# Performance work log

Measured on AMD Instinct MI355X. Metric: run time of the kernel, lower is better.

## Reference

```python
import jax, jax.numpy as jnp
import numpy as np

NS, B, PH = 8, 1024, 12
XS, ZS, RNN = 256, 32, 512
LS, LPS = 8, 2           # len_state, len_pred_state
IN = LPS + ZS + XS       # GRU input size (include_robot=False)
DT = 0.4                 # SingleIntegrator dt


def setup_inputs() -> dict:
    key = jax.random.key(0)
    ks = jax.random.split(key, 16)
    g = lambda k, sh, s=0.05: jax.random.normal(k, sh, dtype=jnp.float32) * s
    N = NS * B
    return {
        "x": g(ks[0], (B, XS), 1.0),
        "x_r_t0": g(ks[1], (B, LS), 1.0),
        "z_stacked": g(ks[2], (NS, B, ZS), 1.0),
        "p0": g(ks[3], (B, 2), 1.0),
        "eps_step": g(ks[4], (PH, N, 2), 1.0),
        "eps_final": g(ks[5], (NS, B, PH, 2), 1.0),
        "W_sa": g(ks[6], (LPS, LS)), "b_sa": jnp.zeros((LPS,), jnp.float32),
        "W_ih": g(ks[7], (3 * RNN, IN)), "b_ih": jnp.zeros((3 * RNN,), jnp.float32),
        "W_hh": g(ks[8], (3 * RNN, RNN)), "b_hh": jnp.zeros((3 * RNN,), jnp.float32),
        "W_h0": g(ks[9], (RNN, ZS + XS)), "b_h0": jnp.zeros((RNN,), jnp.float32),
        "W_mu": g(ks[10], (LPS, RNN)), "b_mu": jnp.zeros((LPS,), jnp.float32),
        "W_ls": g(ks[11], (LPS, RNN), 0.01), "b_ls": jnp.zeros((LPS,), jnp.float32),
        "W_corr": g(ks[12], (1, RNN), 0.01), "b_corr": jnp.zeros((1,), jnp.float32),
        "prediction_horizon": PH,
        "n_samples": NS,
    }


def _gmm_sample(mus, log_sigmas, rho, eps):
    # Reparameterized sample from a single-component 2D correlated Gaussian:
    # a = mu + L @ eps with L = [[sx, 0], [sy*rho, sy*sqrt(1-rho^2)]]
    s = jnp.exp(log_sigmas)
    dx = s[..., 0] * eps[..., 0]
    dy = s[..., 1] * (rho * eps[..., 0]
                      + jnp.sqrt(jnp.clip(1.0 - rho * rho, 1e-5, None)) * eps[..., 1])
    return mus + jnp.stack([dx, dy], axis=-1)


def reference(x, x_r_t0, z_stacked, p0, eps_step, eps_final,
              W_sa, b_sa, W_ih, b_ih, W_hh, b_hh, W_h0, b_h0,
              W_mu, b_mu, W_ls, b_ls, W_corr, b_corr,
              prediction_horizon, n_samples):
    ns, bsz, zs = z_stacked.shape
    z = z_stacked.reshape(-1, zs)                               # [N, z]
    zx = jnp.concatenate([z, jnp.tile(x, (n_samples, 1))], axis=1)  # [N, z+x]
    state0 = zx @ W_h0.T + b_h0                                 # initial_h
    a0 = jnp.tile(x_r_t0 @ W_sa.T + b_sa, (n_samples, 1))       # state_action

    def step(carry, eps_t):
        h, a = carry
        inp = jnp.concatenate([zx, a], axis=1)                  # [N, IN]
        gi = inp @ W_ih.T + b_ih
        gh = h @ W_hh.T + b_hh
        ir, iz, inn = jnp.split(gi, 3, axis=1)
        hr, hz, hn = jnp.split(gh, 3, axis=1)
        r = jax.nn.sigmoid(ir + hr)
        u = jax.nn.sigmoid(iz + hz)
        n = jnp.tanh(inn + r * hn)
        h_new = (1.0 - u) * n + u * h                           # GRUCell
        mus = h_new @ W_mu.T + b_mu                             # [N, 2]
        log_sigmas = h_new @ W_ls.T + b_ls                      # [N, 2]
        corrs = jnp.tanh(h_new @ W_corr.T + b_corr)[:, 0]       # [N]
        a_t = _gmm_sample(mus, log_sigmas, corrs, eps_t)        # gmm.rsample()
        return (h_new, a_t), (mus, log_sigmas, corrs)

    _, (mus, log_sigmas, corrs) = jax.lax.scan(step, (state0, a0), eps_step)
    # [PH, N, .] -> [n_samples, B, PH, .]  (n_components == 1)
    mus = mus.transpose(1, 0, 2).reshape(n_samples, bsz, prediction_horizon, 2)
    log_sigmas = log_sigmas.transpose(1, 0, 2).reshape(n_samples, bsz, prediction_horizon, 2)
    corrs = corrs.transpose(1, 0).reshape(n_samples, bsz, prediction_horizon, 1)
    log_pis = jnp.ones_like(corrs)                              # ones_like path (n_components==1)

    # a_dist.rsample() then SingleIntegrator.integrate_samples
    a_sample = _gmm_sample(mus, log_sigmas, corrs[..., 0], eps_final)
    preds = jnp.cumsum(a_sample, axis=2) * DT + p0[None, :, None, :]
    return (log_pis, mus, log_sigmas, corrs, preds)
```

## Files before the change

kernel.cpp:

```cpp
#include <hip/hip_runtime.h>
#include <hip/hip_bf16.h>
#include <math.h>

#define NSAMP 8
#define BATCH 1024
#define PH 12
#define XS 256
#define ZS 32
#define RNN 512
#define LSZ 8
#define INP 290
#define NTOT 8192
#define DT 0.4f

#define LOGPI_OFF 0
#define MUS_OFF   (NTOT*PH)
#define LSIG_OFF  (MUS_OFF + NTOT*PH*2)
#define CORR_OFF  (LSIG_OFF + NTOT*PH*2)
#define PRED_OFF  (CORR_OFF + NTOT*PH)

typedef float f32x4 __attribute__((ext_vector_type(4)));
typedef __bf16 bf16x8 __attribute__((ext_vector_type(8)));

__device__ __forceinline__ float sigmoid_(float x) {
    return 1.0f / (1.0f + __expf(-x));
}
__device__ __forceinline__ float tanh_(float x) {
    return 1.0f - 2.0f / (__expf(2.0f * x) + 1.0f);
}

__device__ __forceinline__ void async16(const void* g, void* l) {
    __builtin_amdgcn_global_load_lds((const __attribute__((address_space(1))) void*)g,
                                     (__attribute__((address_space(3))) void*)l, 16, 0, 0);
}


__global__ void k_init_a(const float* __restrict__ x_r_t0,
                         const float* __restrict__ W_sa,
                         const float* __restrict__ b_sa,
                         float* __restrict__ a) {
    int n = blockIdx.x * blockDim.x + threadIdx.x;
    if (n >= NTOT) return;
    int b = n & (BATCH - 1);
    float a0 = b_sa[0], a1 = b_sa[1];
#pragma unroll
    for (int k = 0; k < LSZ; ++k) {
        float xv = x_r_t0[b * LSZ + k];
        a0 = fmaf(xv, W_sa[0 * LSZ + k], a0);
        a1 = fmaf(xv, W_sa[1 * LSZ + k], a1);
    }
    a[n * 2 + 0] = a0;
    a[n * 2 + 1] = a1;
}

__global__ void k_cast_zx(const float* __restrict__ z, const float* __restrict__ x,
                          __hip_bfloat16* __restrict__ zx) {
    int n = blockIdx.x, k = threadIdx.x;
    if (k >= 288) return;
    float v = (k < 32) ? z[n * ZS + k] : x[(n & (BATCH - 1)) * XS + (k - 32)];
    zx[(size_t)n * 288 + k] = __float2bfloat16(v);
}

__global__ void k_cast_w(const float* __restrict__ W_h0, const float* __restrict__ W_ih,
                         __hip_bfloat16* __restrict__ Wcat) {
    int r = blockIdx.x, k = threadIdx.x;
    if (k >= 288) return;
    float v = (r < RNN) ? W_h0[r * 288 + k] : W_ih[(size_t)(r - RNN) * INP + k];
    Wcat[(size_t)r * 288 + k] = __float2bfloat16(v);
}

__global__ void k_cast_whh(const float* __restrict__ W, __hip_bfloat16* __restrict__ Wb) {
    int i = blockIdx.x * 256 + threadIdx.x;
    Wb[i] = __float2bfloat16(W[i]);
}

__global__ __launch_bounds__(256, 2) void k_gemm0_mfma(
    const __hip_bfloat16* __restrict__ zx, const __hip_bfloat16* __restrict__ Wcat,
    const float* __restrict__ b_h0, const float* __restrict__ b_ih,
    __hip_bfloat16* __restrict__ h0, __hip_bfloat16* __restrict__ gi)
{
    __shared__ __align__(16) char sA[8192];
    __shared__ __align__(16) char sB[8192];
    const int tid = threadIdx.x;
    const int wv = tid >> 6, lane = tid & 63;
    const int fq = lane >> 4, fr = lane & 15;
    const int wr = wv >> 1, wc = wv & 1;
    const int tile_r = blockIdx.x * 128, tile_c = blockIdx.y * 128;

    f32x4 acc[4][4];
#pragma unroll
    for (int i = 0; i < 4; ++i)
#pragma unroll
        for (int j = 0; j < 4; ++j) acc[i][j] = (f32x4){0.f, 0.f, 0.f, 0.f};

    for (int k0 = 0; k0 < 288; k0 += 32) {
#pragma unroll
        for (int j = 0; j < 2; ++j) {
            int ck = wv * 2 + j;
            int row = ck * 16 + (lane >> 2);
            int slot = lane & 3;
            async16(zx + (size_t)(tile_r + row) * 288 + k0 + ((slot ^ (row & 3)) << 3),
                    sA + ck * 1024 + lane * 16);
        }
#pragma unroll
        for (int j = 0; j < 2; ++j) {
            int ck = wv * 2 + j;
            int row = ck * 16 + (lane >> 2);
            int slot = lane & 3;
            async16(Wcat + (size_t)(tile_c + row) * 288 + k0 + ((slot ^ (row & 3)) << 3),
                    sB + ck * 1024 + lane * 16);
        }
        __syncthreads();
        bf16x8 af[4], bv[4];
#pragma unroll
        for (int i = 0; i < 4; ++i) {
            int r = wr * 64 + i * 16 + fr;
            af[i] = *(const bf16x8*)(sA + r * 64 + ((fq ^ (r & 3)) << 4));
        }
#pragma unroll
        for (int j = 0; j < 4; ++j) {
            int r = wc * 64 + j * 16 + fr;
            bv[j] = *(const bf16x8*)(sB + r * 64 + ((fq ^ (r & 3)) << 4));
        }
#pragma unroll
        for (int i = 0; i < 4; ++i)
#pragma unroll
            for (int j = 0; j < 4; ++j)
                acc[i][j] = __builtin_amdgcn_mfma_f32_16x16x32_bf16(af[i], bv[j], acc[i][j], 0, 0, 0);
        __syncthreads();
    }

#pragma unroll
    for (int jn = 0; jn < 4; ++jn) {
        int cg = tile_c + wc * 64 + jn * 16 + fr;
        float bias = (cg < RNN) ? b_h0[cg] : b_ih[cg - RNN];
#pragma unroll
        for (int i = 0; i < 4; ++i)
#pragma unroll
            for (int q = 0; q < 4; ++q) {
                int rg = tile_r + wr * 64 + i * 16 + fq * 4 + q;
                float v = acc[i][jn][q] + bias;
                if (cg < RNN) h0[(size_t)rg * RNN + cg] = __float2bfloat16(v);
                else          gi[(size_t)rg * 1536 + (cg - RNN)] = __float2bfloat16(v);
            }
    }
}

#define GRU_LDS_A 32768
#define GRU_LDS_BUF 57344
__global__ __launch_bounds__(512, 2) void k_gru_step_mfma(
    const __hip_bfloat16* __restrict__ h, const float* __restrict__ a,
    const __hip_bfloat16* __restrict__ gi,
    const __hip_bfloat16* __restrict__ Whh, const float* __restrict__ b_hh,
    const float* __restrict__ W_ih,
    __hip_bfloat16* __restrict__ h_new)
{
    __shared__ __align__(16) char lds[2][GRU_LDS_BUF];
    const int tid = threadIdx.x;
    const int wv = tid >> 6, lane = tid & 63;
    const int fq = lane >> 4, fr = lane & 15;
    const int wr = wv >> 1, wc = wv & 1;
    const int tile_r = blockIdx.x * 256;
    const int tile_c = blockIdx.y * 64;

    f32x4 acc[3][4][2];
#pragma unroll
    for (int g = 0; g < 3; ++g)
#pragma unroll
        for (int i = 0; i < 4; ++i)
#pragma unroll
            for (int j = 0; j < 2; ++j) acc[g][i][j] = (f32x4){0.f, 0.f, 0.f, 0.f};

    const int lrow = lane >> 2;
    const int slot = (lane & 3) ^ (lrow & 3);

    auto stage = [&](int b, int k0) {
#pragma unroll
        for (int j = 0; j < 7; ++j) {
            int c = wv * 7 + j;
            if (c < 32) {
                int rowgrp = c >> 1, kh = c & 1;
                int row = tile_r + rowgrp * 16 + lrow;
                async16(h + (size_t)row * RNN + k0 + kh * 32 + slot * 8,
                        lds[b] + c * 1024 + lane * 16);
            } else {
                int cp = c - 32;
                int grp = cp >> 1, kh = cp & 1;
                int rB = grp * 16 + lrow;
                int gate = rB >> 6, col = rB & 63;
                async16(Whh + (size_t)(gate * RNN + tile_c + col) * RNN + k0 + kh * 32 + slot * 8,
                        lds[b] + GRU_LDS_A + cp * 1024 + lane * 16);
            }
        }
    };

    auto compute = [&](int b) {
        const char* bufA = lds[b];
        const char* bufB = lds[b] + GRU_LDS_A;
        const int rsw = (fq ^ (fr & 3)) << 4;
#pragma unroll
        for (int ks = 0; ks < 2; ++ks) {
            bf16x8 af[4];
#pragma unroll
            for (int i = 0; i < 4; ++i) {
                int chunk = (wr * 4 + i) * 2 + ks;
                af[i] = *(const bf16x8*)(bufA + chunk * 1024 + fr * 64 + rsw);
            }
            bf16x8 bv[3][2];
#pragma unroll
            for (int g = 0; g < 3; ++g)
#pragma unroll
                for (int j = 0; j < 2; ++j) {
                    int grp = g * 4 + wc * 2 + j;
                    int chunk = grp * 2 + ks;
                    bv[g][j] = *(const bf16x8*)(bufB + chunk * 1024 + fr * 64 + rsw);
                }
#pragma unroll
            for (int g = 0; g < 3; ++g)
#pragma unroll
                for (int i = 0; i < 4; ++i)
#pragma unroll
                    for (int j = 0; j < 2; ++j)
                        acc[g][i][j] = __builtin_amdgcn_mfma_f32_16x16x32_bf16(
                            af[i], bv[g][j], acc[g][i][j], 0, 0, 0);
        }
    };

    stage(0, 0);
    __syncthreads();
    int buf = 0;
#pragma unroll 1
    for (int t = 0; t < 7; ++t) {
        stage(buf ^ 1, (t + 1) * 64);
        compute(buf);
        __syncthreads();
        buf ^= 1;
    }
    compute(buf);

#pragma unroll
    for (int j = 0; j < 2; ++j) {
        const int cg = tile_c + wc * 32 + j * 16 + fr;
        const float bh_r = b_hh[cg], bh_z = b_hh[RNN + cg], bh_n = b_hh[2 * RNN + cg];
        const float wr0 = W_ih[(size_t)cg * INP + 288],             wr1 = W_ih[(size_t)cg * INP + 289];
        const float wz0 = W_ih[(size_t)(RNN + cg) * INP + 288],     wz1 = W_ih[(size_t)(RNN + cg) * INP + 289];
        const float wn0 = W_ih[(size_t)(2 * RNN + cg) * INP + 288], wn1 = W_ih[(size_t)(2 * RNN + cg) * INP + 289];
#pragma unroll
        for (int i = 0; i < 4; ++i)
#pragma unroll
            for (int q = 0; q < 4; ++q) {
                const int rg = tile_r + wr * 64 + i * 16 + fq * 4 + q;
                const float2 av = *(const float2*)&a[rg * 2];
                const float gr = __bfloat162float(gi[(size_t)rg * 1536 + cg])
                                 + av.x * wr0 + av.y * wr1 + acc[0][i][j][q] + bh_r;
                const float gz = __bfloat162float(gi[(size_t)rg * 1536 + RNN + cg])
                                 + av.x * wz0 + av.y * wz1 + acc[1][i][j][q] + bh_z;
                const float gn = __bfloat162float(gi[(size_t)rg * 1536 + 2 * RNN + cg])
                                 + av.x * wn0 + av.y * wn1;
                const float r_ = sigmoid_(gr);
                const float u_ = sigmoid_(gz);
                const float n_ = tanh_(gn + r_ * (acc[2][i][j][q] + bh_n));
                const float hv = __bfloat162float(h[(size_t)rg * RNN + cg]);
                h_new[(size_t)rg * RNN + cg] = __float2bfloat16((1.0f - u_) * n_ + u_ * hv);
            }
    }
}

__global__ __launch_bounds__(256) void k_heads(
    const __hip_bfloat16* __restrict__ h_new,
    const float* __restrict__ W_mu, const float* __restrict__ b_mu,
    const float* __restrict__ W_ls, const float* __restrict__ b_ls,
    const float* __restrict__ W_corr, const float* __restrict__ b_corr,
    const float* __restrict__ eps_step_t,
    float* __restrict__ out, float* __restrict__ a, int t)
{
    const int wid = (blockIdx.x * blockDim.x + threadIdx.x) >> 6;
    const int lane = threadIdx.x & 63;
    if (wid >= NTOT) return;
    const int kbase = lane * 8;
    float hv[8];
    {
        uint4 v = *reinterpret_cast<const uint4*>(&h_new[(size_t)wid * RNN + kbase]);
        unsigned uu[4] = {v.x, v.y, v.z, v.w};
#pragma unroll
        for (int p = 0; p < 4; ++p) {
            hv[2 * p]     = __uint_as_float(uu[p] << 16);
            hv[2 * p + 1] = __uint_as_float(uu[p] & 0xffff0000u);
        }
    }
    float s0 = 0.f, s1 = 0.f, s2 = 0.f, s3 = 0.f, s4 = 0.f;
#pragma unroll
    for (int q = 0; q < 8; ++q) {
        int k = kbase + q;
        s0 = fmaf(hv[q], W_mu[k], s0);
        s1 = fmaf(hv[q], W_mu[RNN + k], s1);
        s2 = fmaf(hv[q], W_ls[k], s2);
        s3 = fmaf(hv[q], W_ls[RNN + k], s3);
        s4 = fmaf(hv[q], W_corr[k], s4);
    }
#pragma unroll
    for (int m = 32; m >= 1; m >>= 1) {
        s0 += __shfl_xor(s0, m, 64);
        s1 += __shfl_xor(s1, m, 64);
        s2 += __shfl_xor(s2, m, 64);
        s3 += __shfl_xor(s3, m, 64);
        s4 += __shfl_xor(s4, m, 64);
    }
    if (lane == 0) {
        const int n = wid;
        const float mu0 = s0 + b_mu[0], mu1 = s1 + b_mu[1];
        const float ls0 = s2 + b_ls[0], ls1 = s3 + b_ls[1];
        const float rho = tanh_(s4 + b_corr[0]);
        out[MUS_OFF + (n * PH + t) * 2 + 0] = mu0;
        out[MUS_OFF + (n * PH + t) * 2 + 1] = mu1;
        out[LSIG_OFF + (n * PH + t) * 2 + 0] = ls0;
        out[LSIG_OFF + (n * PH + t) * 2 + 1] = ls1;
        out[CORR_OFF + n * PH + t] = rho;
        const float e0 = eps_step_t[n * 2 + 0], e1 = eps_step_t[n * 2 + 1];
        const float sg0 = __expf(ls0), sg1 = __expf(ls1);
        a[n * 2 + 0] = mu0 + sg0 * e0;
        a[n * 2 + 1] = mu1 + sg1 * (rho * e0 + sqrtf(fmaxf(1e-5f, 1.0f - rho * rho)) * e1);
    }
}

__global__ void k_final(const float* __restrict__ p0,
                        const float* __restrict__ eps_final,
                        float* __restrict__ out)
{
    int n = blockIdx.x * blockDim.x + threadIdx.x;
    if (n >= NTOT) return;
    const int b = n & (BATCH - 1);
    const float px = p0[b * 2 + 0], py = p0[b * 2 + 1];
    float cx = 0.f, cy = 0.f;
#pragma unroll
    for (int t = 0; t < PH; ++t) {
        const float mu0 = out[MUS_OFF + (n * PH + t) * 2 + 0];
        const float mu1 = out[MUS_OFF + (n * PH + t) * 2 + 1];
        const float ls0 = out[LSIG_OFF + (n * PH + t) * 2 + 0];
        const float ls1 = out[LSIG_OFF + (n * PH + t) * 2 + 1];
        const float rho = out[CORR_OFF + n * PH + t];
        const float e0 = eps_final[(n * PH + t) * 2 + 0];
        const float e1 = eps_final[(n * PH + t) * 2 + 1];
        const float sg0 = __expf(ls0), sg1 = __expf(ls1);
        cx += mu0 + sg0 * e0;
        cy += mu1 + sg1 * (rho * e0 + sqrtf(fmaxf(1e-5f, 1.0f - rho * rho)) * e1);
        out[PRED_OFF + (n * PH + t) * 2 + 0] = cx * DT + px;
        out[PRED_OFF + (n * PH + t) * 2 + 1] = cy * DT + py;
        out[LOGPI_OFF + n * PH + t] = 1.0f;
    }
}

extern "C" void kernel_launch(void* const* d_in, const int* in_sizes, int n_in,
                              void* d_out, int out_size, void* d_ws, size_t ws_size,
                              hipStream_t stream) {
    const float* x        = (const float*)d_in[0];
    const float* x_r_t0   = (const float*)d_in[1];
    const float* z        = (const float*)d_in[2];
    const float* p0       = (const float*)d_in[3];
    const float* eps_step = (const float*)d_in[4];
    const float* eps_fin  = (const float*)d_in[5];
    const float* W_sa     = (const float*)d_in[6];
    const float* b_sa     = (const float*)d_in[7];
    const float* W_ih     = (const float*)d_in[8];
    const float* b_ih     = (const float*)d_in[9];
    const float* W_hh     = (const float*)d_in[10];
    const float* b_hh     = (const float*)d_in[11];
    const float* W_h0     = (const float*)d_in[12];
    const float* b_h0     = (const float*)d_in[13];
    const float* W_mu     = (const float*)d_in[14];
    const float* b_mu     = (const float*)d_in[15];
    const float* W_ls     = (const float*)d_in[16];
    const float* b_ls     = (const float*)d_in[17];
    const float* W_corr   = (const float*)d_in[18];
    const float* b_corr   = (const float*)d_in[19];

    char* wp = (char*)d_ws;
    float* a            = (float*)wp;          wp += (size_t)NTOT * 2 * 4;
    __hip_bfloat16* zxb = (__hip_bfloat16*)wp; wp += (size_t)NTOT * 288 * 2;
    __hip_bfloat16* Wcat= (__hip_bfloat16*)wp; wp += (size_t)2048 * 288 * 2;
    __hip_bfloat16* Whhb= (__hip_bfloat16*)wp; wp += (size_t)1536 * RNN * 2;
    __hip_bfloat16* h0  = (__hip_bfloat16*)wp; wp += (size_t)NTOT * RNN * 2;
    __hip_bfloat16* h1  = (__hip_bfloat16*)wp; wp += (size_t)NTOT * RNN * 2;
    __hip_bfloat16* gi  = (__hip_bfloat16*)wp; wp += (size_t)NTOT * 1536 * 2;
    float* out = (float*)d_out;

    k_init_a<<<dim3(NTOT / 256), dim3(256), 0, stream>>>(x_r_t0, W_sa, b_sa, a);
    k_cast_zx<<<dim3(NTOT), dim3(320), 0, stream>>>(z, x, zxb);
    k_cast_w<<<dim3(2048), dim3(320), 0, stream>>>(W_h0, W_ih, Wcat);
    k_cast_whh<<<dim3(1536 * RNN / 256), dim3(256), 0, stream>>>(W_hh, Whhb);
    k_gemm0_mfma<<<dim3(64, 16), dim3(256), 0, stream>>>(zxb, Wcat, b_h0, b_ih, h0, gi);

    __hip_bfloat16* hc = h0;
    __hip_bfloat16* hn = h1;
    for (int t = 0; t < PH; ++t) {
        k_gru_step_mfma<<<dim3(NTOT / 256, RNN / 64), dim3(512), 0, stream>>>(
            hc, a, gi, Whhb, b_hh, W_ih, hn);
        k_heads<<<dim3(NTOT * 64 / 256), dim3(256), 0, stream>>>(
            hn, W_mu, b_mu, W_ls, b_ls, W_corr, b_corr,
            eps_step + (size_t)t * NTOT * 2, out, a, t);
        __hip_bfloat16* tmp = hc; hc = hn; hn = tmp;
    }
    k_final<<<dim3(NTOT / 256), dim3(256), 0, stream>>>(p0, eps_fin, out);
}
```

Baseline: 422.5 us.

## Fuse head projections into GRU step epilogue via per-slice partial sums

The GRU step kernel now computes the mu, log-sigma and corr projections of the new hidden state in its epilogue. It reduces across the 16 columns of each fragment with shuffles and writes 16 per-slice partials per row to a workspace buffer. A light k_heads_fin kernel then sums the partials, applies biases, writes the outputs and samples the next action. This removes the extra pass that re-read the full bf16 hidden state every step, at the cost of more epilogue registers (launch bounds relaxed to 1 block) and an extra partials buffer round-trip.

```diff
diff --git a/kernel.cpp b/kernel.cpp
--- a/kernel.cpp
+++ b/kernel.cpp
@@ -148,12 +148,14 @@
 
 #define GRU_LDS_A 32768
 #define GRU_LDS_BUF 57344
-__global__ __launch_bounds__(512, 2) void k_gru_step_mfma(
+__global__ __launch_bounds__(512, 1) void k_gru_step_mfma(
     const __hip_bfloat16* __restrict__ h, const float* __restrict__ a,
     const __hip_bfloat16* __restrict__ gi,
     const __hip_bfloat16* __restrict__ Whh, const float* __restrict__ b_hh,
     const float* __restrict__ W_ih,
-    __hip_bfloat16* __restrict__ h_new)
+    const float* __restrict__ W_mu, const float* __restrict__ W_ls,
+    const float* __restrict__ W_corr,
+    __hip_bfloat16* __restrict__ h_new, float* __restrict__ partial)
 {
     __shared__ __align__(16) char lds[2][GRU_LDS_BUF];
     const int tid = threadIdx.x;
@@ -238,89 +240,95 @@
     }
     compute(buf);
 
+    int cg[2];
+    float bhr[2], bhz[2], bhn[2];
+    float wr0[2], wr1[2], wz0[2], wz1[2], wn0[2], wn1[2];
+    float wmu0[2], wmu1[2], wls0[2], wls1[2], wcor[2];
 #pragma unroll
     for (int j = 0; j < 2; ++j) {
-        const int cg = tile_c + wc * 32 + j * 16 + fr;
-        const float bh_r = b_hh[cg], bh_z = b_hh[RNN + cg], bh_n = b_hh[2 * RNN + cg];
-        const float wr0 = W_ih[(size_t)cg * INP + 288],             wr1 = W_ih[(size_t)cg * INP + 289];
-        const float wz0 = W_ih[(size_t)(RNN + cg) * INP + 288],     wz1 = W_ih[(size_t)(RNN + cg) * INP + 289];
-        const float wn0 = W_ih[(size_t)(2 * RNN + cg) * INP + 288], wn1 = W_ih[(size_t)(2 * RNN + cg) * INP + 289];
-#pragma unroll
-        for (int i = 0; i < 4; ++i)
-#pragma unroll
-            for (int q = 0; q < 4; ++q) {
-                const int rg = tile_r + wr * 64 + i * 16 + fq * 4 + q;
-                const float2 av = *(const float2*)&a[rg * 2];
-                const float gr = __bfloat162float(gi[(size_t)rg * 1536 + cg])
-                                 + av.x * wr0 + av.y * wr1 + acc[0][i][j][q] + bh_r;
-                const float gz = __bfloat162float(gi[(size_t)rg * 1536 + RNN + cg])
-                                 + av.x * wz0 + av.y * wz1 + acc[1][i][j][q] + bh_z;
-                const float gn = __bfloat162float(gi[(size_t)rg * 1536 + 2 * RNN + cg])
-                                 + av.x * wn0 + av.y * wn1;
+        const int c = tile_c + wc * 32 + j * 16 + fr;
+        cg[j] = c;
+        bhr[j] = b_hh[c]; bhz[j] = b_hh[RNN + c]; bhn[j] = b_hh[2 * RNN + c];
+        wr0[j] = W_ih[(size_t)c * INP + 288];             wr1[j] = W_ih[(size_t)c * INP + 289];
+        wz0[j] = W_ih[(size_t)(RNN + c) * INP + 288];     wz1[j] = W_ih[(size_t)(RNN + c) * INP + 289];
+        wn0[j] = W_ih[(size_t)(2 * RNN + c) * INP + 288]; wn1[j] = W_ih[(size_t)(2 * RNN + c) * INP + 289];
+        wmu0[j] = W_mu[c]; wmu1[j] = W_mu[RNN + c];
+        wls0[j] = W_ls[c]; wls1[j] = W_ls[RNN + c];
+        wcor[j] = W_corr[c];
+    }
+    const int slice = (blockIdx.y << 1) + wc;
+
+#pragma unroll
+    for (int i = 0; i < 4; ++i)
+#pragma unroll
+        for (int q = 0; q < 4; ++q) {
+            const int rg = tile_r + wr * 64 + i * 16 + fq * 4 + q;
+            const float2 av = *(const float2*)&a[rg * 2];
+            float p0 = 0.f, p1 = 0.f, p2 = 0.f, p3 = 0.f, p4 = 0.f;
+#pragma unroll
+            for (int j = 0; j < 2; ++j) {
+                const float gr = __bfloat162float(gi[(size_t)rg * 1536 + cg[j]])
+                                 + av.x * wr0[j] + av.y * wr1[j] + acc[0][i][j][q] + bhr[j];
+                const float gz = __bfloat162float(gi[(size_t)rg * 1536 + RNN + cg[j]])
+                                 + av.x * wz0[j] + av.y * wz1[j] + acc[1][i][j][q] + bhz[j];
+                const float gn = __bfloat162float(gi[(size_t)rg * 1536 + 2 * RNN + cg[j]])
+                                 + av.x * wn0[j] + av.y * wn1[j];
                 const float r_ = sigmoid_(gr);
                 const float u_ = sigmoid_(gz);
-                const float n_ = tanh_(gn + r_ * (acc[2][i][j][q] + bh_n));
-                const float hv = __bfloat162float(h[(size_t)rg * RNN + cg]);
-                h_new[(size_t)rg * RNN + cg] = __float2bfloat16((1.0f - u_) * n_ + u_ * hv);
-            }
-    }
-}
-
-__global__ __launch_bounds__(256) void k_heads(
-    const __hip_bfloat16* __restrict__ h_new,
-    const float* __restrict__ W_mu, const float* __restrict__ b_mu,
-    const float* __restrict__ W_ls, const float* __restrict__ b_ls,
-    const float* __restrict__ W_corr, const float* __restrict__ b_corr,
+                const float n_ = tanh_(gn + r_ * (acc[2][i][j][q] + bhn[j]));
+                const float hv = __bfloat162float(h[(size_t)rg * RNN + cg[j]]);
+                const float hnew = (1.0f - u_) * n_ + u_ * hv;
+                h_new[(size_t)rg * RNN + cg[j]] = __float2bfloat16(hnew);
+                p0 = fmaf(hnew, wmu0[j], p0);
+                p1 = fmaf(hnew, wmu1[j], p1);
+                p2 = fmaf(hnew, wls0[j], p2);
+                p3 = fmaf(hnew, wls1[j], p3);
+                p4 = fmaf(hnew, wcor[j], p4);
+            }
+#pragma unroll
+            for (int m = 1; m <= 8; m <<= 1) {
+                p0 += __shfl_xor(p0, m, 64);
+                p1 += __shfl_xor(p1, m, 64);
+                p2 += __shfl_xor(p2, m, 64);
+                p3 += __shfl_xor(p3, m, 64);
+                p4 += __shfl_xor(p4, m, 64);
+            }
+            if (fr == 0) {
+                float* pr = partial + ((size_t)rg * 16 + slice) * 5;
+                pr[0] = p0; pr[1] = p1; pr[2] = p2; pr[3] = p3; pr[4] = p4;
+            }
+        }
+}
+
+__global__ __launch_bounds__(256) void k_heads_fin(
+    const float* __restrict__ partial,
+    const float* __restrict__ b_mu, const float* __restrict__ b_ls,
+    const float* __restrict__ b_corr,
     const float* __restrict__ eps_step_t,
     float* __restrict__ out, float* __restrict__ a, int t)
 {
-    const int wid = (blockIdx.x * blockDim.x + threadIdx.x) >> 6;
-    const int lane = threadIdx.x & 63;
-    if (wid >= NTOT) return;
-    const int kbase = lane * 8;
-    float hv[8];
-    {
-        uint4 v = *reinterpret_cast<const uint4*>(&h_new[(size_t)wid * RNN + kbase]);
-        unsigned uu[4] = {v.x, v.y, v.z, v.w};
-#pragma unroll
-        for (int p = 0; p < 4; ++p) {
-            hv[2 * p]     = __uint_as_float(uu[p] << 16);
-            hv[2 * p + 1] = __uint_as_float(uu[p] & 0xffff0000u);
-        }
-    }
+    const int n = blockIdx.x * blockDim.x + threadIdx.x;
+    if (n >= NTOT) return;
+    const float* pr = partial + (size_t)n * 80;
     float s0 = 0.f, s1 = 0.f, s2 = 0.f, s3 = 0.f, s4 = 0.f;
 #pragma unroll
-    for (int q = 0; q < 8; ++q) {
-        int k = kbase + q;
-        s0 = fmaf(hv[q], W_mu[k], s0);
-        s1 = fmaf(hv[q], W_mu[RNN + k], s1);
-        s2 = fmaf(hv[q], W_ls[k], s2);
-        s3 = fmaf(hv[q], W_ls[RNN + k], s3);
-        s4 = fmaf(hv[q], W_corr[k], s4);
-    }
-#pragma unroll
-    for (int m = 32; m >= 1; m >>= 1) {
-        s0 += __shfl_xor(s0, m, 64);
-        s1 += __shfl_xor(s1, m, 64);
-        s2 += __shfl_xor(s2, m, 64);
-        s3 += __shfl_xor(s3, m, 64);
-        s4 += __shfl_xor(s4, m, 64);
-    }
-    if (lane == 0) {
-        const int n = wid;
-        const float mu0 = s0 + b_mu[0], mu1 = s1 + b_mu[1];
-        const float ls0 = s2 + b_ls[0], ls1 = s3 + b_ls[1];
-        const float rho = tanh_(s4 + b_corr[0]);
-        out[MUS_OFF + (n * PH + t) * 2 + 0] = mu0;
-        out[MUS_OFF + (n * PH + t) * 2 + 1] = mu1;
-        out[LSIG_OFF + (n * PH + t) * 2 + 0] = ls0;
-        out[LSIG_OFF + (n * PH + t) * 2 + 1] = ls1;
-        out[CORR_OFF + n * PH + t] = rho;
-        const float e0 = eps_step_t[n * 2 + 0], e1 = eps_step_t[n * 2 + 1];
-        const float sg0 = __expf(ls0), sg1 = __expf(ls1);
-        a[n * 2 + 0] = mu0 + sg0 * e0;
-        a[n * 2 + 1] = mu1 + sg1 * (rho * e0 + sqrtf(fmaxf(1e-5f, 1.0f - rho * rho)) * e1);
-    }
+    for (int sl = 0; sl < 16; ++sl) {
+        const float4 v0 = *reinterpret_cast<const float4*>(pr + sl * 5);
+        s0 += v0.x; s1 += v0.y; s2 += v0.z; s3 += v0.w;
+        s4 += pr[sl * 5 + 4];
+    }
+    const float mu0 = s0 + b_mu[0], mu1 = s1 + b_mu[1];
+    const float ls0 = s2 + b_ls[0], ls1 = s3 + b_ls[1];
+    const float rho = tanh_(s4 + b_corr[0]);
+    out[MUS_OFF + (n * PH + t) * 2 + 0] = mu0;
+    out[MUS_OFF + (n * PH + t) * 2 + 1] = mu1;
+    out[LSIG_OFF + (n * PH + t) * 2 + 0] = ls0;
+    out[LSIG_OFF + (n * PH + t) * 2 + 1] = ls1;
+    out[CORR_OFF + n * PH + t] = rho;
+    const float e0 = eps_step_t[n * 2 + 0], e1 = eps_step_t[n * 2 + 1];
+    const float sg0 = __expf(ls0), sg1 = __expf(ls1);
+    a[n * 2 + 0] = mu0 + sg0 * e0;
+    a[n * 2 + 1] = mu1 + sg1 * (rho * e0 + sqrtf(fmaxf(1e-5f, 1.0f - rho * rho)) * e1);
 }
 
 __global__ void k_final(const float* __restrict__ p0,
@@ -376,6 +384,7 @@
 
     char* wp = (char*)d_ws;
     float* a            = (float*)wp;          wp += (size_t)NTOT * 2 * 4;
+    float* partial      = (float*)wp;          wp += (size_t)NTOT * 16 * 5 * 4;
     __hip_bfloat16* zxb = (__hip_bfloat16*)wp; wp += (size_t)NTOT * 288 * 2;
     __hip_bfloat16* Wcat= (__hip_bfloat16*)wp; wp += (size_t)2048 * 288 * 2;
     __hip_bfloat16* Whhb= (__hip_bfloat16*)wp; wp += (size_t)1536 * RNN * 2;
@@ -394,9 +403,9 @@
     __hip_bfloat16* hn = h1;
     for (int t = 0; t < PH; ++t) {
         k_gru_step_mfma<<<dim3(NTOT / 256, RNN / 64), dim3(512), 0, stream>>>(
-            hc, a, gi, Whhb, b_hh, W_ih, hn);
-        k_heads<<<dim3(NTOT * 64 / 256), dim3(256), 0, stream>>>(
-            hn, W_mu, b_mu, W_ls, b_ls, W_corr, b_corr,
+            hc, a, gi, Whhb, b_hh, W_ih, W_mu, W_ls, W_corr, hn, partial);
+        k_heads_fin<<<dim3(NTOT / 256), dim3(256), 0, stream>>>(
+            partial, b_mu, b_ls, b_corr,
             eps_step + (size_t)t * NTOT * 2, out, a, t);
         __hip_bfloat16* tmp = hc; hc = hn; hn = tmp;
     }
```

Result: slower. 467.4 us (+10.6%).

## Store input-gate preactivations in per-thread fragment layout for contiguous GRU loads

Applied to the files above, without the earlier changes.

The first GEMM now writes the gi preactivations in a layout permuted to match each GRU-step thread's accumulator fragment, so each thread reads its 96 bf16 values with twelve 16-byte loads at kernel start. This replaces strided 2-byte gathers from a row-major gi in the GRU epilogue. The gathers happened in all 12 steps. In exchange it adds 48 registers of prefetched data per thread, which may pressure occupancy under launch_bounds(512,2). It also hard-codes the GRU grid and tile mapping into the GEMM epilogue.

```diff
diff --git a/kernel.cpp b/kernel.cpp
--- a/kernel.cpp
+++ b/kernel.cpp
@@ -28,6 +28,10 @@
 __device__ __forceinline__ float tanh_(float x) {
     return 1.0f - 2.0f / (__expf(2.0f * x) + 1.0f);
 }
+__device__ __forceinline__ unsigned short f2bfu(float v) {
+    __hip_bfloat16 b = __float2bfloat16(v);
+    return __builtin_bit_cast(unsigned short, b);
+}
 
 __device__ __forceinline__ void async16(const void* g, void* l) {
     __builtin_amdgcn_global_load_lds((const __attribute__((address_space(1))) void*)g,
@@ -77,7 +81,7 @@
 __global__ __launch_bounds__(256, 2) void k_gemm0_mfma(
     const __hip_bfloat16* __restrict__ zx, const __hip_bfloat16* __restrict__ Wcat,
     const float* __restrict__ b_h0, const float* __restrict__ b_ih,
-    __hip_bfloat16* __restrict__ h0, __hip_bfloat16* __restrict__ gi)
+    __hip_bfloat16* __restrict__ h0, unsigned short* __restrict__ giP)
 {
     __shared__ __align__(16) char sA[8192];
     __shared__ __align__(16) char sB[8192];
@@ -132,17 +136,44 @@
 
 #pragma unroll
     for (int jn = 0; jn < 4; ++jn) {
-        int cg = tile_c + wc * 64 + jn * 16 + fr;
-        float bias = (cg < RNN) ? b_h0[cg] : b_ih[cg - RNN];
-#pragma unroll
-        for (int i = 0; i < 4; ++i)
-#pragma unroll
-            for (int q = 0; q < 4; ++q) {
-                int rg = tile_r + wr * 64 + i * 16 + fq * 4 + q;
-                float v = acc[i][jn][q] + bias;
-                if (cg < RNN) h0[(size_t)rg * RNN + cg] = __float2bfloat16(v);
-                else          gi[(size_t)rg * 1536 + (cg - RNN)] = __float2bfloat16(v);
+        const int cg_full = tile_c + wc * 64 + jn * 16 + fr;
+        if (cg_full < RNN) {
+            const float bias = b_h0[cg_full];
+#pragma unroll
+            for (int i = 0; i < 4; ++i)
+#pragma unroll
+                for (int q = 0; q < 4; ++q) {
+                    int rg = tile_r + wr * 64 + i * 16 + fq * 4 + q;
+                    h0[(size_t)rg * RNN + cg_full] = __float2bfloat16(acc[i][jn][q] + bias);
+                }
+        } else {
+            const int cp = cg_full - RNN;
+            const float bias = b_ih[cp];
+            const int g = cp >> 9;
+            const int cgm = cp & 511;
+            const int by = cgm >> 6;
+            const int wcg = (cgm >> 5) & 1;
+            const int jg = (cgm >> 4) & 1;
+            const int frg = cgm & 15;
+#pragma unroll
+            for (int i = 0; i < 4; ++i) {
+                const int rg = tile_r + wr * 64 + i * 16 + fq * 4;
+                const int bxg = rg >> 8;
+                const int r255 = rg & 255;
+                const int wrg = r255 >> 6;
+                const int ig = (r255 >> 4) & 3;
+                const int fqg = (r255 >> 2) & 3;
+                const int tidg = (wrg * 2 + wcg) * 64 + fqg * 16 + frg;
+                const size_t base = ((size_t)(bxg * 8 + by) * 512 + tidg) * 96
+                                    + (jg * 3 + g) * 16 + ig * 4;
+                ushort4 pk;
+                pk.x = f2bfu(acc[i][jn][0] + bias);
+                pk.y = f2bfu(acc[i][jn][1] + bias);
+                pk.z = f2bfu(acc[i][jn][2] + bias);
+                pk.w = f2bfu(acc[i][jn][3] + bias);
+                *reinterpret_cast<ushort4*>(giP + base) = pk;
             }
+        }
     }
 }
 
@@ -150,7 +181,7 @@
 #define GRU_LDS_BUF 57344
 __global__ __launch_bounds__(512, 2) void k_gru_step_mfma(
     const __hip_bfloat16* __restrict__ h, const float* __restrict__ a,
-    const __hip_bfloat16* __restrict__ gi,
+    const unsigned short* __restrict__ giP,
     const __hip_bfloat16* __restrict__ Whh, const float* __restrict__ b_hh,
     const float* __restrict__ W_ih,
     __hip_bfloat16* __restrict__ h_new)
@@ -162,6 +193,12 @@
     const int wr = wv >> 1, wc = wv & 1;
     const int tile_r = blockIdx.x * 256;
     const int tile_c = blockIdx.y * 64;
+
+    const unsigned short* pg = giP + ((size_t)(blockIdx.x * 8 + blockIdx.y) * 512 + tid) * 96;
+    bf16x8 gv[12];
+#pragma unroll
+    for (int e = 0; e < 12; ++e)
+        gv[e] = *reinterpret_cast<const bf16x8*>(pg + e * 8);
 
     f32x4 acc[3][4][2];
 #pragma unroll
@@ -250,12 +287,14 @@
 #pragma unroll
             for (int q = 0; q < 4; ++q) {
                 const int rg = tile_r + wr * 64 + i * 16 + fq * 4 + q;
+                const int idx = i * 4 + q;
+                const int half = idx >> 3, lidx = idx & 7;
                 const float2 av = *(const float2*)&a[rg * 2];
-                const float gr = __bfloat162float(gi[(size_t)rg * 1536 + cg])
+                const float gr = __bfloat162float(gv[(j * 3 + 0) * 2 + half][lidx])
                                  + av.x * wr0 + av.y * wr1 + acc[0][i][j][q] + bh_r;
-                const float gz = __bfloat162float(gi[(size_t)rg * 1536 + RNN + cg])
+                const float gz = __bfloat162float(gv[(j * 3 + 1) * 2 + half][lidx])
                                  + av.x * wz0 + av.y * wz1 + acc[1][i][j][q] + bh_z;
-                const float gn = __bfloat162float(gi[(size_t)rg * 1536 + 2 * RNN + cg])
+                const float gn = __bfloat162float(gv[(j * 3 + 2) * 2 + half][lidx])
                                  + av.x * wn0 + av.y * wn1;
                 const float r_ = sigmoid_(gr);
                 const float u_ = sigmoid_(gz);
@@ -381,20 +420,20 @@
     __hip_bfloat16* Whhb= (__hip_bfloat16*)wp; wp += (size_t)1536 * RNN * 2;
     __hip_bfloat16* h0  = (__hip_bfloat16*)wp; wp += (size_t)NTOT * RNN * 2;
     __hip_bfloat16* h1  = (__hip_bfloat16*)wp; wp += (size_t)NTOT * RNN * 2;
-    __hip_bfloat16* gi  = (__hip_bfloat16*)wp; wp += (size_t)NTOT * 1536 * 2;
+    unsigned short* giP = (unsigned short*)wp; wp += (size_t)NTOT * 1536 * 2;
     float* out = (float*)d_out;
 
     k_init_a<<<dim3(NTOT / 256), dim3(256), 0, stream>>>(x_r_t0, W_sa, b_sa, a);
     k_cast_zx<<<dim3(NTOT), dim3(320), 0, stream>>>(z, x, zxb);
     k_cast_w<<<dim3(2048), dim3(320), 0, stream>>>(W_h0, W_ih, Wcat);
     k_cast_whh<<<dim3(1536 * RNN / 256), dim3(256), 0, stream>>>(W_hh, Whhb);
-    k_gemm0_mfma<<<dim3(64, 16), dim3(256), 0, stream>>>(zxb, Wcat, b_h0, b_ih, h0, gi);
+    k_gemm0_mfma<<<dim3(64, 16), dim3(256), 0, stream>>>(zxb, Wcat, b_h0, b_ih, h0, giP);
 
     __hip_bfloat16* hc = h0;
     __hip_bfloat16* hn = h1;
     for (int t = 0; t < PH; ++t) {
         k_gru_step_mfma<<<dim3(NTOT / 256, RNN / 64), dim3(512), 0, stream>>>(
-            hc, a, gi, Whhb, b_hh, W_ih, hn);
+            hc, a, giP, Whhb, b_hh, W_ih, hn);
         k_heads<<<dim3(NTOT * 64 / 256), dim3(256), 0, stream>>>(
             hn, W_mu, b_mu, W_ls, b_ls, W_corr, b_corr,
             eps_step + (size_t)t * NTOT * 2, out, a, t);
```

Measured after the change: 426.0 us. About the same (+0.8%).
